# Performance work log

Hardware: AMD Instinct MI355X
Metric: run time of the kernel (lower is better)

## Reference

```python
import jax, jax.numpy as jnp
import numpy as np
import math

HEADS = 8
HID = 32
MODES = 8
IN_CH = 4
SEQ = 32
B = 2
H = 64
W = 64


def spectral_conv(x, wr, wi):
    # x: [N, Cin, H, W]; w: [Cin, Cout, m, m] complex (low rfft2 modes only)
    n, _, h, w = x.shape
    m = wr.shape[2]
    xf = jnp.fft.rfft2(x)  # [N, Cin, H, W//2+1] complex64
    of = jnp.einsum('bixy,ioxy->boxy', xf[:, :, :m, :m], wr + 1j * wi)
    out_ft = jnp.zeros((n, wr.shape[1], h, w // 2 + 1), dtype=of.dtype)
    out_ft = out_ft.at[:, :, :m, :m].set(of)
    return jnp.fft.irfft2(out_ft, s=(h, w))


def conv1x1(x, w, b):
    # x: [N, Cin, H, W], w: [Cout, Cin], b: [Cout]
    return jnp.einsum('bchw,oc->bohw', x, w) + b[None, :, None, None]


def setup_inputs() -> dict:
    key = jax.random.key(0)
    ks = jax.random.split(key, 16)
    hd = HEADS * HID
    s = 0.02
    inp = {
        'v': jax.random.normal(ks[0], (B, SEQ, IN_CH, H, W), dtype=jnp.float32),
        'qwr': jax.random.normal(ks[1], (IN_CH, hd, MODES, MODES), dtype=jnp.float32) * s,
        'qwi': jax.random.normal(ks[2], (IN_CH, hd, MODES, MODES), dtype=jnp.float32) * s,
        'kwr': jax.random.normal(ks[3], (IN_CH, hd, MODES, MODES), dtype=jnp.float32) * s,
        'kwi': jax.random.normal(ks[4], (IN_CH, hd, MODES, MODES), dtype=jnp.float32) * s,
        'vwr': jax.random.normal(ks[5], (IN_CH, hd, MODES, MODES), dtype=jnp.float32) * s,
        'vwi': jax.random.normal(ks[6], (IN_CH, hd, MODES, MODES), dtype=jnp.float32) * s,
        'u1wr': jax.random.normal(ks[7], (hd, HID, MODES, MODES), dtype=jnp.float32) * s,
        'u1wi': jax.random.normal(ks[8], (hd, HID, MODES, MODES), dtype=jnp.float32) * s,
        'u2wr': jax.random.normal(ks[9], (HID, IN_CH, MODES, MODES), dtype=jnp.float32) * s,
        'u2wi': jax.random.normal(ks[10], (HID, IN_CH, MODES, MODES), dtype=jnp.float32) * s,
        's1w': jax.random.normal(ks[11], (HID, hd), dtype=jnp.float32) * s,
        's1b': jnp.zeros((HID,), dtype=jnp.float32),
        's2w': jax.random.normal(ks[12], (IN_CH, HID), dtype=jnp.float32) * s,
        's2b': jnp.zeros((IN_CH,), dtype=jnp.float32),
    }
    return inp


def reference(v, qwr, qwi, kwr, kwi, vwr, vwi, u1wr, u1wi, u2wr, u2wi, s1w, s1b, s2w, s2b):
    b, s, c, h, w = v.shape
    scale = 1.0 / math.sqrt(HID / HEADS)
    vr = v.reshape(b * s, c, h, w)
    embed = (b, HEADS, s, -1, h, w)  # same raw row-major reshape as torch
    q = spectral_conv(vr, qwr, qwi).reshape(embed)
    k = spectral_conv(vr, kwr, kwi).reshape(embed)
    val = spectral_conv(vr, vwr, vwi).reshape(embed)
    # inner products over channel dim, then dx^2-weighted spatial integral
    ip = jnp.einsum('bhsdrc,bhtdrc->bhstrc', q, k) * scale
    dx = 1.0 / h
    l2 = jnp.sum(ip, axis=(-2, -1)) * (dx * dx)  # [b, h, s1, s2]
    A = jax.nn.softmax(l2, axis=-1)
    u = jnp.einsum('bhst,bhtdrc->bhsdrc', A, val)
    u = jnp.transpose(u, (0, 2, 1, 3, 4, 5)).reshape(b * s, HEADS * u.shape[3], h, w)
    # SimpleFNO: gelu(conv1) + skip1, then conv2 + skip2
    x1 = jax.nn.gelu(spectral_conv(u, u1wr, u1wi), approximate=False) + conv1x1(u, s1w, s1b)
    x2 = spectral_conv(x1, u2wr, u2wi) + conv1x1(x1, s2w, s2b)
    return x2.reshape(b, s, c, h, w)
```

## Files before the change

### kernel.cpp

```cpp
#include <hip/hip_runtime.h>
#include <math.h>

#define HEADS 8
#define HIDC  32
#define MODES 8
#define IN_CH 4
#define SEQ   32
#define NS    64
#define HD    256
#define NM    64
#define NPIX  4096
#define TWO_PI_D 6.283185307179586476925286766559

__device__ __forceinline__ float2 f2(float a, float b){ return make_float2(a,b); }

__global__ void twiddle_kernel(float2* __restrict__ Etab){
  int t = threadIdx.x;
  int a = t >> 3, b = t & 7;
  double sv, cv; sincos(TWO_PI_D * ((a*b) & 63) / 64.0, &sv, &cv);
  Etab[t] = f2((float)cv, (float)sv);
}

__global__ __launch_bounds__(256) void fwd_dft_kernel(const float* __restrict__ src,
                                                      const float2* __restrict__ Etab,
                                                      float2* __restrict__ dst){
  int f = blockIdx.x, tid = threadIdx.x;
  __shared__ float  s_fld[64*68];
  __shared__ float2 s_e[64][8];
  __shared__ float2 s_a1[64][8];
  for (int e = tid; e < 512; e += 256) ((float2*)s_e)[e] = Etab[e];
  const float4* f4 = (const float4*)(src + (size_t)f*NPIX);
  for (int k = tid; k < 1024; k += 256){
    float4 v = f4[k];
    int y = k >> 4, x4 = (k & 15)*4;
    float* row = &s_fld[y*68 + x4];
    row[0]=v.x; row[1]=v.y; row[2]=v.z; row[3]=v.w;
  }
  __syncthreads();
  for (int o = tid; o < 512; o += 256){
    int y = o >> 3, kx = o & 7;
    const float4* row = (const float4*)&s_fld[y*68];
    float sr = 0.f, si = 0.f;
    for (int x4 = 0; x4 < 16; ++x4){
      float4 v = row[x4];
      int xb = x4*4;
      float2 c0 = s_e[xb+0][kx], c1 = s_e[xb+1][kx];
      float2 c2 = s_e[xb+2][kx], c3 = s_e[xb+3][kx];
      sr += v.x*c0.x + v.y*c1.x + v.z*c2.x + v.w*c3.x;
      si -= v.x*c0.y + v.y*c1.y + v.z*c2.y + v.w*c3.y;
    }
    s_a1[y][kx] = f2(sr, si);
  }
  __syncthreads();
  if (tid < 64){
    int ky = tid >> 3, kx = tid & 7;
    float sr = 0.f, si = 0.f;
    for (int y = 0; y < 64; ++y){
      float2 a = s_a1[y][kx];
      float2 cs = s_e[y][ky];
      sr += a.x*cs.x + a.y*cs.y;
      si += a.y*cs.x - a.x*cs.y;
    }
    dst[(size_t)f*NM + tid] = f2(sr, si);
  }
}

__global__ __launch_bounds__(256) void gram_kernel(const float* __restrict__ qwr, const float* __restrict__ qwi,
                                                   const float* __restrict__ kwr, const float* __restrict__ kwi,
                                                   float2* __restrict__ G2, float* __restrict__ Gdc){
  int m = blockIdx.x, tid = threadIdx.x;
  __shared__ float qsr[4][257], qsi[4][257], ksr[4][257], ksi[4][257];
  for (int k = tid; k < 1024; k += 256){
    int i = k >> 8, c = k & 255;
    size_t a = ((size_t)(i*256 + c))*64 + m;
    qsr[i][c] = qwr[a]; qsi[i][c] = qwi[a];
    ksr[i][c] = kwr[a]; ksi[i][c] = kwi[a];
  }
  __syncthreads();
  int kx = m & 7, ky = m >> 3;
  float w = (kx >= 1) ? 2.0f : ((ky >= 1) ? 0.5f : 0.0f);
  for (int e = tid; e < 1024; e += 256){
    int P = e >> 7, T = (e >> 4) & 7, i = (e >> 2) & 3, j = e & 3;
    float grr=0.f, gri=0.f, gir=0.f, gii=0.f;
    for (int d = 0; d < 32; ++d){
      float ar = qsr[i][P*32+d], ai = qsi[i][P*32+d];
      float br = ksr[j][T*32+d], bi = ksi[j][T*32+d];
      grr += ar*br; gri += ar*bi; gir += ai*br; gii += ai*bi;
    }
    G2[(size_t)(((m*8+P)*4+i)*4+j)*8 + T] = f2(w*(grr+gii), w*(gir-gri));
    if (m == 0){
      int o = ((P*4+i)*4+j)*8 + T;
      Gdc[o] = grr; Gdc[1024+o] = gri; Gdc[2048+o] = gir; Gdc[3072+o] = gii;
    }
  }
}

__global__ __launch_bounds__(256) void attn_kernel(const float2* __restrict__ Vf,
                                                   const float2* __restrict__ G2,
                                                   const float* __restrict__ Gdc,
                                                   float* __restrict__ A){
  int bx = blockIdx.x;
  int s = bx & 31;
  int base = ((bx >> 8) * 32) + (((bx >> 5) & 7) * 4);
  int tid = threadIdx.x;
  int t = tid & 31, mc = tid >> 5;
  __shared__ float2 s_vf[4][IN_CH][64];
  __shared__ float  s_part[8][33];
  for (int k = tid; k < 4*IN_CH*64; k += 256){
    int m = k & 63, c = (k>>6)&3, smp = k>>8;
    s_vf[smp][c][m] = Vf[((size_t)(base+smp)*IN_CH + c)*NM + m];
  }
  __syncthreads();
  int sg = s >> 3, P = s & 7;
  int tg = t >> 3, T = t & 7;
  float acc = 0.f;
  for (int mm = 0; mm < 8; ++mm){
    int m = mc*8 + mm;
    const float2* g = G2 + (size_t)((m*8+P)*16)*8 + T;
    float sub = 0.f;
    for (int i = 0; i < 4; ++i){
      float2 a = s_vf[sg][i][m];
      for (int j = 0; j < 4; ++j){
        float2 b = s_vf[tg][j][m];
        float zr = a.x*b.x + a.y*b.y;
        float zi = a.y*b.x - a.x*b.y;
        float2 gv = g[(size_t)(i*4+j)*8];
        sub += zr*gv.x - zi*gv.y;
      }
    }
    acc += sub;
  }
  if (mc == 0){
    float sub = 0.f;
    for (int i = 0; i < 4; ++i){
      float2 a = s_vf[sg][i][0];
      for (int j = 0; j < 4; ++j){
        float2 b = s_vf[tg][j][0];
        int o = ((P*4+i)*4+j)*8 + T;
        sub += a.x*b.x*Gdc[o] - a.x*b.y*Gdc[1024+o]
             - a.y*b.x*Gdc[2048+o] + a.y*b.y*Gdc[3072+o];
      }
    }
    acc += sub;
  }
  s_part[mc][t] = acc;
  __syncthreads();
  if (tid < 32){
    float l2 = 0.f;
    for (int k = 0; k < 8; ++k) l2 += s_part[k][tid];
    l2 *= 0.5f / (4096.0f * 4096.0f);
    float mx = l2;
    for (int off = 16; off; off >>= 1) mx = fmaxf(mx, __shfl_xor(mx, off, 32));
    float e = expf(l2 - mx);
    float sm = e;
    for (int off = 16; off; off >>= 1) sm += __shfl_xor(sm, off, 32);
    A[(size_t)bx*32 + tid] = e / sm;
  }
}

__global__ __launch_bounds__(256) void uspec_kernel(const float2* __restrict__ Vf,
                                                    const float* __restrict__ vwr, const float* __restrict__ vwi,
                                                    const float* __restrict__ A,
                                                    float2* __restrict__ Uf){
  int bid = blockIdx.x;
  int mg = bid & 31, hh = (bid >> 5) & 7, b = bid >> 8;
  int m0 = mg*2;
  int nbase = b*32 + hh*4;
  int tid = threadIdx.x;
  __shared__ float2 s_vw[4][2][256];
  __shared__ float2 s_vv[4][2][256];
  __shared__ float  s_A[32][33];
  __shared__ float2 s_vf[4][4][2];
  for (int k = tid; k < 2048; k += 256){
    int i = k >> 9, mm = (k >> 8) & 1, c = k & 255;
    size_t a = ((size_t)i*256 + c)*64 + m0 + mm;
    s_vw[i][mm][c] = f2(vwr[a], vwi[a]);
  }
  for (int k = tid; k < 1024; k += 256)
    s_A[k>>5][k&31] = A[(size_t)((b*8+hh)*32 + (k>>5))*32 + (k&31)];
  if (tid < 32){
    int smp = tid >> 3, i = (tid >> 1) & 3, mm = tid & 1;
    s_vf[smp][i][mm] = Vf[((size_t)(nbase+smp)*4 + i)*64 + m0 + mm];
  }
  __syncthreads();
  for (int k = tid; k < 2048; k += 256){
    int smp = k >> 9, mm = (k >> 8) & 1, c = k & 255;
    float sr = 0.f, si = 0.f;
    for (int i = 0; i < 4; ++i){
      float2 v = s_vf[smp][i][mm];
      float2 w = s_vw[i][mm][c];
      sr += v.x*w.x - v.y*w.y;
      si += v.x*w.y + v.y*w.x;
    }
    s_vv[smp][mm][c] = f2(sr, si);
  }
  __syncthreads();
  int sg = tid >> 5, d = tid & 31;
  float2 acc[4][2];
  for (int ss = 0; ss < 4; ++ss)
    for (int mm = 0; mm < 2; ++mm) acc[ss][mm] = f2(0.f, 0.f);
  for (int tt = 0; tt < 32; ++tt){
    int tg = tt >> 3, c = (tt & 7)*32 + d;
    float a0 = s_A[sg*4+0][tt], a1 = s_A[sg*4+1][tt];
    float a2 = s_A[sg*4+2][tt], a3 = s_A[sg*4+3][tt];
    for (int mm = 0; mm < 2; ++mm){
      float2 v = s_vv[tg][mm][c];
      acc[0][mm].x += a0*v.x; acc[0][mm].y += a0*v.y;
      acc[1][mm].x += a1*v.x; acc[1][mm].y += a1*v.y;
      acc[2][mm].x += a2*v.x; acc[2][mm].y += a2*v.y;
      acc[3][mm].x += a3*v.x; acc[3][mm].y += a3*v.y;
    }
  }
  for (int ss = 0; ss < 4; ++ss){
    int n = b*32 + sg*4 + ss;
    for (int mm = 0; mm < 2; ++mm)
      Uf[((size_t)n*64 + m0 + mm)*256 + hh*32 + d] = acc[ss][mm];
  }
}

__global__ __launch_bounds__(256) void u1t_kernel(const float* __restrict__ u1wr,
                                                  const float* __restrict__ u1wi,
                                                  float4* __restrict__ u1wT){
  int t = blockIdx.x*256 + threadIdx.x;
  int o1 = t & 31, c = (t>>5) & 255, m = t >> 13;
  float pr = ((m & 7)==0 && m) ? 0.5f : 1.0f;
  float pi = m ? pr : 0.0f;
  size_t src = ((size_t)c*32 + o1)*64 + m;
  float wr = u1wr[src], wi = u1wi[src];
  u1wT[t] = make_float4(pr*wr, pi*wi, pr*wi, pi*wr);
}

__global__ __launch_bounds__(128) void mix1_kernel(const float2* __restrict__ Uf,
                                                   const float4* __restrict__ u1wT,
                                                   const float* __restrict__ s1w,
                                                   float2* __restrict__ U1f, float2* __restrict__ S1f){
  int n = blockIdx.x >> 4, mg = blockIdx.x & 15, m0 = mg*4;
  int tid = threadIdx.x;
  __shared__ float2 s_u[4][256];
  for (int k = tid; k < 1024; k += 128){
    int mm = k >> 8, c = k & 255;
    s_u[mm][c] = Uf[((size_t)n*64 + m0 + mm)*256 + c];
  }
  __syncthreads();
  int o1 = tid & 31, mm = tid >> 5;
  int m = m0 + mm;
  const float4* wp = u1wT + (size_t)m*256*32 + o1;
  const float* swp = s1w + o1*256;
  float2 au = f2(0.f,0.f), asv = f2(0.f,0.f);
  #pragma unroll 8
  for (int c = 0; c < 256; ++c){
    float2 u = s_u[mm][c];
    float4 w = wp[(size_t)c*32];
    float sw = swp[c];
    au.x  += u.x*w.x - u.y*w.y;
    au.y  += u.x*w.z + u.y*w.w;
    asv.x += u.x*sw;
    asv.y += u.y*sw;
  }
  size_t ob = ((size_t)n*32 + o1)*64 + m;
  U1f[ob] = au; S1f[ob] = asv;
}

__global__ __launch_bounds__(256) void xg_kernel(const float2* __restrict__ Etab,
                                                 const float2* __restrict__ U1f,
                                                 float2* __restrict__ Xg){
  int f = blockIdx.x, tid = threadIdx.x;
  __shared__ float2 s_e[64][8];
  __shared__ float2 s_gu[64];
  __shared__ float2 s_tu[64][8];
  __shared__ float  s_fld[64*68];
  __shared__ float2 s_a1[64][8];
  for (int e = tid; e < 512; e += 256) ((float2*)s_e)[e] = Etab[e];
  if (tid < 64) s_gu[tid] = U1f[(size_t)f*NM + tid];
  __syncthreads();
  for (int o = tid; o < 512; o += 256){
    int y = o >> 3, kx = o & 7;
    float wf = (kx ? 2.0f : 1.0f) * (1.0f/4096.0f);
    float ar=0.f, ai=0.f;
    for (int ky = 0; ky < 8; ++ky){
      float2 cs = s_e[y][ky];
      float2 gu = s_gu[ky*8+kx];
      ar += gu.x*cs.x - gu.y*cs.y;
      ai += gu.x*cs.y + gu.y*cs.x;
    }
    s_tu[y][kx] = f2(ar*wf, ai*wf);
  }
  __syncthreads();
  int xx = tid & 63;
  float2 ce[8];
  #pragma unroll
  for (int k = 0; k < 8; ++k) ce[k] = s_e[xx][k];
  for (int i = 0; i < 16; ++i){
    int p = i*256 + tid;
    int y = p >> 6;
    const float4* tp = (const float4*)&s_tu[y][0];
    float4 t0 = tp[0], t1 = tp[1], t2 = tp[2], t3 = tp[3];
    float vu = t0.x*ce[0].x - t0.y*ce[0].y + t0.z*ce[1].x - t0.w*ce[1].y
             + t1.x*ce[2].x - t1.y*ce[2].y + t1.z*ce[3].x - t1.w*ce[3].y
             + t2.x*ce[4].x - t2.y*ce[4].y + t2.z*ce[5].x - t2.w*ce[5].y
             + t3.x*ce[6].x - t3.y*ce[6].y + t3.z*ce[7].x - t3.w*ce[7].y;
    float g = 0.5f * vu * (1.0f + erff(vu * 0.70710678f));
    s_fld[y*68 + xx] = g;
  }
  __syncthreads();
  for (int o = tid; o < 512; o += 256){
    int y = o >> 3, kx = o & 7;
    const float4* row = (const float4*)&s_fld[y*68];
    float sr = 0.f, si = 0.f;
    for (int x4 = 0; x4 < 16; ++x4){
      float4 v = row[x4];
      int xb = x4*4;
      float2 c0 = s_e[xb+0][kx], c1 = s_e[xb+1][kx];
      float2 c2 = s_e[xb+2][kx], c3 = s_e[xb+3][kx];
      sr += v.x*c0.x + v.y*c1.x + v.z*c2.x + v.w*c3.x;
      si -= v.x*c0.y + v.y*c1.y + v.z*c2.y + v.w*c3.y;
    }
    s_a1[y][kx] = f2(sr, si);
  }
  __syncthreads();
  if (tid < 64){
    int ky = tid >> 3, kx = tid & 7;
    float sr = 0.f, si = 0.f;
    for (int y = 0; y < 64; ++y){
      float2 a = s_a1[y][kx];
      float2 cs = s_e[y][ky];
      sr += a.x*cs.x + a.y*cs.y;
      si += a.y*cs.x - a.x*cs.y;
    }
    Xg[(size_t)f*NM + tid] = f2(sr, si);
  }
}

__global__ __launch_bounds__(256) void final_kernel(const float2* __restrict__ Etab,
                                                    const float2* __restrict__ U1f,
                                                    const float2* __restrict__ S1f,
                                                    const float2* __restrict__ Xg,
                                                    const float* __restrict__ u2wr, const float* __restrict__ u2wi,
                                                    const float* __restrict__ s1b,
                                                    const float* __restrict__ s2w, const float* __restrict__ s2b,
                                                    float* __restrict__ out){
  int n = blockIdx.x >> 4, tile = blockIdx.x & 15, y0 = tile*4;
  int tid = threadIdx.x;
  __shared__ float2 s_e[64][8];
  __shared__ float2 s_u1[32][64];
  __shared__ float2 s_T[32][4][8];
  __shared__ float2 s_os[4][64];
  __shared__ float2 s_tmp[4][4][8];
  __shared__ float  s_w2[128], s_s1b[32], s_b2[4];
  for (int e = tid; e < 512; e += 256) ((float2*)s_e)[e] = Etab[e];
  for (int k = tid; k < 2048; k += 256) ((float2*)s_u1)[k] = U1f[(size_t)n*2048 + k];
  if (tid < 128) s_w2[tid] = s2w[tid];
  else if (tid < 160) s_s1b[tid-128] = s1b[tid-128];
  else if (tid < 164) s_b2[tid-160] = s2b[tid-160];
  __syncthreads();
  for (int e = tid; e < 1024; e += 256){
    int c = e >> 5, yy = (e >> 3) & 3, kx = e & 7;
    int y = y0 + yy;
    float wf = (kx ? 2.0f : 1.0f) * (1.0f/4096.0f);
    float ar = 0.f, ai = 0.f;
    for (int ky = 0; ky < 8; ++ky){
      float2 cs = s_e[y][ky];
      float2 g = s_u1[c][ky*8+kx];
      ar += g.x*cs.x - g.y*cs.y;
      ai += g.x*cs.y + g.y*cs.x;
    }
    s_T[c][yy][kx] = f2(ar*wf, ai*wf);
  }
  {
    int o2 = tid >> 6, m = tid & 63;
    float prm = ((m & 7)==0 && m) ? 0.5f : 1.0f;
    float pim = m ? prm : 0.0f;
    float dc = (m == 0) ? 4096.0f : 0.0f;
    float cr = 0.f, ci = 0.f;
    for (int o1 = 0; o1 < 32; ++o1){
      float2 xg = Xg[((size_t)n*32 + o1)*NM + m];
      float2 sf = S1f[((size_t)n*32 + o1)*NM + m];
      float Xr = xg.x + sf.x*prm + dc*s_s1b[o1];
      float Xi = xg.y + sf.y*pim;
      size_t wb = ((size_t)(o1*IN_CH + o2))*NM + m;
      float wr = u2wr[wb], wi = u2wi[wb];
      float sw = s_w2[o2*32 + o1];
      cr += Xr*wr - Xi*wi + sw*sf.x;
      ci += Xr*wi + Xi*wr + sw*sf.y;
    }
    s_os[o2][m] = f2(cr, ci);
  }
  __syncthreads();
  if (tid < 128){
    int o2 = tid >> 5, yy = (tid >> 3) & 3, kx = tid & 7;
    int y = y0 + yy;
    float wf = (kx ? 2.0f : 1.0f) * (1.0f/4096.0f);
    float tr=0.f, ti=0.f;
    for (int ky = 0; ky < 8; ++ky){
      float2 cs = s_e[y][ky];
      float2 g = s_os[o2][ky*8+kx];
      tr += g.x*cs.x - g.y*cs.y;
      ti += g.x*cs.y + g.y*cs.x;
    }
    s_tmp[o2][yy][kx] = f2(tr*wf, ti*wf);
  }
  __syncthreads();
  int yy = tid >> 6, xx = tid & 63;
  float2 ce[8];
  #pragma unroll
  for (int k = 0; k < 8; ++k) ce[k] = s_e[xx][k];
  float a0 = s_b2[0], a1 = s_b2[1], a2 = s_b2[2], a3 = s_b2[3];
  for (int c = 0; c < 32; ++c){
    float b = s_s1b[c];
    a0 += s_w2[c]*b; a1 += s_w2[32+c]*b; a2 += s_w2[64+c]*b; a3 += s_w2[96+c]*b;
  }
  for (int c = 0; c < 32; ++c){
    const float4* tp = (const float4*)&s_T[c][yy][0];
    float4 t0 = tp[0], t1 = tp[1], t2 = tp[2], t3 = tp[3];
    float vu = t0.x*ce[0].x - t0.y*ce[0].y + t0.z*ce[1].x - t0.w*ce[1].y
             + t1.x*ce[2].x - t1.y*ce[2].y + t1.z*ce[3].x - t1.w*ce[3].y
             + t2.x*ce[4].x - t2.y*ce[4].y + t2.z*ce[5].x - t2.w*ce[5].y
             + t3.x*ce[6].x - t3.y*ce[6].y + t3.z*ce[7].x - t3.w*ce[7].y;
    float g = 0.5f * vu * (1.0f + erff(vu * 0.70710678f));
    a0 += s_w2[c]*g; a1 += s_w2[32+c]*g; a2 += s_w2[64+c]*g; a3 += s_w2[96+c]*g;
  }
  float sp[4];
  #pragma unroll
  for (int o2 = 0; o2 < 4; ++o2){
    const float4* tp = (const float4*)&s_tmp[o2][yy][0];
    float4 t0 = tp[0], t1 = tp[1], t2 = tp[2], t3 = tp[3];
    sp[o2] = t0.x*ce[0].x - t0.y*ce[0].y + t0.z*ce[1].x - t0.w*ce[1].y
           + t1.x*ce[2].x - t1.y*ce[2].y + t1.z*ce[3].x - t1.w*ce[3].y
           + t2.x*ce[4].x - t2.y*ce[4].y + t2.z*ce[5].x - t2.w*ce[5].y
           + t3.x*ce[6].x - t3.y*ce[6].y + t3.z*ce[7].x - t3.w*ce[7].y;
  }
  int p = (y0 + yy)*64 + xx;
  float* ob = out + (size_t)n*IN_CH*NPIX;
  ob[p]          = a0 + sp[0];
  ob[NPIX + p]   = a1 + sp[1];
  ob[2*NPIX + p] = a2 + sp[2];
  ob[3*NPIX + p] = a3 + sp[3];
}

extern "C" void kernel_launch(void* const* d_in, const int* in_sizes, int n_in,
                              void* d_out, int out_size, void* d_ws, size_t ws_size,
                              hipStream_t stream) {
  (void)in_sizes; (void)n_in; (void)out_size; (void)ws_size;
  const float* v    = (const float*)d_in[0];
  const float* qwr  = (const float*)d_in[1];
  const float* qwi  = (const float*)d_in[2];
  const float* kwr  = (const float*)d_in[3];
  const float* kwi  = (const float*)d_in[4];
  const float* vwr  = (const float*)d_in[5];
  const float* vwi  = (const float*)d_in[6];
  const float* u1wr = (const float*)d_in[7];
  const float* u1wi = (const float*)d_in[8];
  const float* u2wr = (const float*)d_in[9];
  const float* u2wi = (const float*)d_in[10];
  const float* s1w  = (const float*)d_in[11];
  const float* s1b  = (const float*)d_in[12];
  const float* s2w  = (const float*)d_in[13];
  const float* s2b  = (const float*)d_in[14];
  float* out = (float*)d_out;

  float* ws = (float*)d_ws;
  size_t off = 0;
  float2* Etab =(float2*)(ws + off); off += 1024;
  float2* Vf   = (float2*)(ws + off); off += (size_t)NS*IN_CH*NM*2;
  float2* G2   = (float2*)(ws + off); off += (size_t)65536*2;
  float*  Gdc  =          (ws + off); off += 4096;
  float*  A    =          (ws + off); off += 16384;
  float2* Uf   = (float2*)(ws + off); off += (size_t)NS*NM*HD*2;
  float2* U1f  = (float2*)(ws + off); off += (size_t)NS*HIDC*NM*2;
  float2* S1f  = (float2*)(ws + off); off += (size_t)NS*HIDC*NM*2;
  float2* Xg   = (float2*)(ws + off); off += (size_t)NS*HIDC*NM*2;
  float4* u1wT = (float4*)(ws + off); off += (size_t)524288*4;

  twiddle_kernel<<<1, 512, 0, stream>>>(Etab);
  fwd_dft_kernel<<<NS*IN_CH, 256, 0, stream>>>(v, Etab, Vf);
  gram_kernel<<<64, 256, 0, stream>>>(qwr, qwi, kwr, kwi, G2, Gdc);
  u1t_kernel<<<2048, 256, 0, stream>>>(u1wr, u1wi, u1wT);
  attn_kernel<<<512, 256, 0, stream>>>(Vf, G2, Gdc, A);
  uspec_kernel<<<512, 256, 0, stream>>>(Vf, vwr, vwi, A, Uf);
  mix1_kernel<<<1024, 128, 0, stream>>>(Uf, u1wT, s1w, U1f, S1f);
  xg_kernel<<<NS*HIDC, 256, 0, stream>>>(Etab, U1f, Xg);
  final_kernel<<<NS*16, 256, 0, stream>>>(Etab, U1f, S1f, Xg, u2wr, u2wi, s1b, s2w, s2b, out);
}
```

Baseline: 222.0 us.

## Batch samples in mix1/xg, pre-transpose value weights, coalesce u1 transpose

mix1 now processes four samples per block, so each u1 weight load is reused across four samples and the grid shrinks fourfold. xg handles two fields per block, sharing the twiddle load and reusing the s_tu buffer for the stage-one DFT output. A new v1t kernel transposes the value spectral weights so uspec loads them contiguously, and u1t now reads coalesced instead of writing coalesced. fwd_dft uses 512 threads with one output per thread. The trade-offs are fewer blocks and higher register and shared-memory use per block, plus one extra small launch.

```diff
diff --git a/kernel.cpp b/kernel.cpp
--- a/kernel.cpp
+++ b/kernel.cpp
@@ -21,23 +21,24 @@
   Etab[t] = f2((float)cv, (float)sv);
 }
 
-__global__ __launch_bounds__(256) void fwd_dft_kernel(const float* __restrict__ src,
+__global__ __launch_bounds__(512) void fwd_dft_kernel(const float* __restrict__ src,
                                                       const float2* __restrict__ Etab,
                                                       float2* __restrict__ dst){
   int f = blockIdx.x, tid = threadIdx.x;
   __shared__ float  s_fld[64*68];
   __shared__ float2 s_e[64][8];
   __shared__ float2 s_a1[64][8];
-  for (int e = tid; e < 512; e += 256) ((float2*)s_e)[e] = Etab[e];
+  if (tid < 512) ((float2*)s_e)[tid] = Etab[tid];
   const float4* f4 = (const float4*)(src + (size_t)f*NPIX);
-  for (int k = tid; k < 1024; k += 256){
+  for (int k = tid; k < 1024; k += 512){
     float4 v = f4[k];
     int y = k >> 4, x4 = (k & 15)*4;
     float* row = &s_fld[y*68 + x4];
     row[0]=v.x; row[1]=v.y; row[2]=v.z; row[3]=v.w;
   }
   __syncthreads();
-  for (int o = tid; o < 512; o += 256){
+  {
+    int o = tid;
     int y = o >> 3, kx = o & 7;
     const float4* row = (const float4*)&s_fld[y*68];
     float sr = 0.f, si = 0.f;
@@ -158,8 +159,16 @@
   }
 }
 
+__global__ __launch_bounds__(256) void v1t_kernel(const float* __restrict__ vwr,
+                                                  const float* __restrict__ vwi,
+                                                  float2* __restrict__ vwT){
+  int t = blockIdx.x*256 + threadIdx.x;
+  int m = t & 63, r = t >> 6, i = r >> 8, c = r & 255;
+  vwT[((size_t)m*256 + c)*4 + i] = f2(vwr[t], vwi[t]);
+}
+
 __global__ __launch_bounds__(256) void uspec_kernel(const float2* __restrict__ Vf,
-                                                    const float* __restrict__ vwr, const float* __restrict__ vwi,
+                                                    const float2* __restrict__ vwT,
                                                     const float* __restrict__ A,
                                                     float2* __restrict__ Uf){
   int bid = blockIdx.x;
@@ -172,9 +181,8 @@
   __shared__ float  s_A[32][33];
   __shared__ float2 s_vf[4][4][2];
   for (int k = tid; k < 2048; k += 256){
-    int i = k >> 9, mm = (k >> 8) & 1, c = k & 255;
-    size_t a = ((size_t)i*256 + c)*64 + m0 + mm;
-    s_vw[i][mm][c] = f2(vwr[a], vwi[a]);
+    int mm = k >> 10, c = (k >> 2) & 255, i = k & 3;
+    s_vw[i][mm][c] = vwT[(size_t)m0*1024 + k];
   }
   for (int k = tid; k < 1024; k += 256)
     s_A[k>>5][k&31] = A[(size_t)((b*8+hh)*32 + (k>>5))*32 + (k&31)];
@@ -222,90 +230,105 @@
                                                   const float* __restrict__ u1wi,
                                                   float4* __restrict__ u1wT){
   int t = blockIdx.x*256 + threadIdx.x;
-  int o1 = t & 31, c = (t>>5) & 255, m = t >> 13;
+  int m = t & 63, r = t >> 6, c = r >> 5, o1 = r & 31;
   float pr = ((m & 7)==0 && m) ? 0.5f : 1.0f;
   float pi = m ? pr : 0.0f;
-  size_t src = ((size_t)c*32 + o1)*64 + m;
-  float wr = u1wr[src], wi = u1wi[src];
-  u1wT[t] = make_float4(pr*wr, pi*wi, pr*wi, pi*wr);
+  float wr = u1wr[t], wi = u1wi[t];
+  u1wT[((size_t)m*256 + c)*32 + o1] = make_float4(pr*wr, pi*wi, pr*wi, pi*wr);
 }
 
 __global__ __launch_bounds__(128) void mix1_kernel(const float2* __restrict__ Uf,
                                                    const float4* __restrict__ u1wT,
                                                    const float* __restrict__ s1w,
                                                    float2* __restrict__ U1f, float2* __restrict__ S1f){
-  int n = blockIdx.x >> 4, mg = blockIdx.x & 15, m0 = mg*4;
+  int bid = blockIdx.x;
+  int n0 = (bid >> 4)*4, mg = bid & 15, m0 = mg*4;
   int tid = threadIdx.x;
-  __shared__ float2 s_u[4][256];
-  for (int k = tid; k < 1024; k += 128){
-    int mm = k >> 8, c = k & 255;
-    s_u[mm][c] = Uf[((size_t)n*64 + m0 + mm)*256 + c];
+  __shared__ float2 s_u[4][4][256];
+  for (int k = tid; k < 4096; k += 128){
+    int smp = k >> 10, mm = (k >> 8) & 3, c = k & 255;
+    s_u[smp][mm][c] = Uf[((size_t)(n0+smp)*64 + m0 + mm)*256 + c];
   }
   __syncthreads();
   int o1 = tid & 31, mm = tid >> 5;
   int m = m0 + mm;
-  const float4* wp = u1wT + (size_t)m*256*32 + o1;
+  const float4* wp = u1wT + (size_t)m*8192 + o1;
   const float* swp = s1w + o1*256;
-  float2 au = f2(0.f,0.f), asv = f2(0.f,0.f);
-  #pragma unroll 8
+  float2 au[4], asv[4];
+  #pragma unroll
+  for (int s = 0; s < 4; ++s){ au[s] = f2(0.f,0.f); asv[s] = f2(0.f,0.f); }
   for (int c = 0; c < 256; ++c){
-    float2 u = s_u[mm][c];
     float4 w = wp[(size_t)c*32];
     float sw = swp[c];
-    au.x  += u.x*w.x - u.y*w.y;
-    au.y  += u.x*w.z + u.y*w.w;
-    asv.x += u.x*sw;
-    asv.y += u.y*sw;
-  }
-  size_t ob = ((size_t)n*32 + o1)*64 + m;
-  U1f[ob] = au; S1f[ob] = asv;
+    #pragma unroll
+    for (int s = 0; s < 4; ++s){
+      float2 u = s_u[s][mm][c];
+      au[s].x  += u.x*w.x - u.y*w.y;
+      au[s].y  += u.x*w.z + u.y*w.w;
+      asv[s].x += u.x*sw;
+      asv[s].y += u.y*sw;
+    }
+  }
+  #pragma unroll
+  for (int s = 0; s < 4; ++s){
+    size_t ob = ((size_t)(n0+s)*32 + o1)*64 + m;
+    U1f[ob] = au[s]; S1f[ob] = asv[s];
+  }
 }
 
 __global__ __launch_bounds__(256) void xg_kernel(const float2* __restrict__ Etab,
                                                  const float2* __restrict__ U1f,
                                                  float2* __restrict__ Xg){
-  int f = blockIdx.x, tid = threadIdx.x;
+  int f0 = blockIdx.x*2, tid = threadIdx.x;
   __shared__ float2 s_e[64][8];
-  __shared__ float2 s_gu[64];
-  __shared__ float2 s_tu[64][8];
-  __shared__ float  s_fld[64*68];
-  __shared__ float2 s_a1[64][8];
+  __shared__ float2 s_gu[2][64];
+  __shared__ float2 s_tu[2][64][8];
+  __shared__ float  s_fld[2][64*68];
   for (int e = tid; e < 512; e += 256) ((float2*)s_e)[e] = Etab[e];
-  if (tid < 64) s_gu[tid] = U1f[(size_t)f*NM + tid];
-  __syncthreads();
-  for (int o = tid; o < 512; o += 256){
-    int y = o >> 3, kx = o & 7;
+  if (tid < 128) ((float2*)s_gu)[tid] = U1f[(size_t)f0*NM + tid];
+  __syncthreads();
+  for (int o = tid; o < 1024; o += 256){
+    int fl = o >> 9, r = o & 511, y = r >> 3, kx = r & 7;
     float wf = (kx ? 2.0f : 1.0f) * (1.0f/4096.0f);
     float ar=0.f, ai=0.f;
     for (int ky = 0; ky < 8; ++ky){
       float2 cs = s_e[y][ky];
-      float2 gu = s_gu[ky*8+kx];
+      float2 gu = s_gu[fl][ky*8+kx];
       ar += gu.x*cs.x - gu.y*cs.y;
       ai += gu.x*cs.y + gu.y*cs.x;
     }
-    s_tu[y][kx] = f2(ar*wf, ai*wf);
+    s_tu[fl][y][kx] = f2(ar*wf, ai*wf);
   }
   __syncthreads();
   int xx = tid & 63;
   float2 ce[8];
   #pragma unroll
   for (int k = 0; k < 8; ++k) ce[k] = s_e[xx][k];
+  #pragma unroll 2
   for (int i = 0; i < 16; ++i){
-    int p = i*256 + tid;
-    int y = p >> 6;
-    const float4* tp = (const float4*)&s_tu[y][0];
-    float4 t0 = tp[0], t1 = tp[1], t2 = tp[2], t3 = tp[3];
-    float vu = t0.x*ce[0].x - t0.y*ce[0].y + t0.z*ce[1].x - t0.w*ce[1].y
-             + t1.x*ce[2].x - t1.y*ce[2].y + t1.z*ce[3].x - t1.w*ce[3].y
-             + t2.x*ce[4].x - t2.y*ce[4].y + t2.z*ce[5].x - t2.w*ce[5].y
-             + t3.x*ce[6].x - t3.y*ce[6].y + t3.z*ce[7].x - t3.w*ce[7].y;
-    float g = 0.5f * vu * (1.0f + erff(vu * 0.70710678f));
-    s_fld[y*68 + xx] = g;
-  }
-  __syncthreads();
-  for (int o = tid; o < 512; o += 256){
-    int y = o >> 3, kx = o & 7;
-    const float4* row = (const float4*)&s_fld[y*68];
+    int p = i*256 + tid, y = p >> 6;
+    const float4* tp0 = (const float4*)&s_tu[0][y][0];
+    const float4* tp1 = (const float4*)&s_tu[1][y][0];
+    float4 a0=tp0[0], a1=tp0[1], a2=tp0[2], a3=tp0[3];
+    float4 b0=tp1[0], b1=tp1[1], b2=tp1[2], b3=tp1[3];
+    float v0 = a0.x*ce[0].x - a0.y*ce[0].y + a0.z*ce[1].x - a0.w*ce[1].y
+             + a1.x*ce[2].x - a1.y*ce[2].y + a1.z*ce[3].x - a1.w*ce[3].y
+             + a2.x*ce[4].x - a2.y*ce[4].y + a2.z*ce[5].x - a2.w*ce[5].y
+             + a3.x*ce[6].x - a3.y*ce[6].y + a3.z*ce[7].x - a3.w*ce[7].y;
+    float v1 = b0.x*ce[0].x - b0.y*ce[0].y + b0.z*ce[1].x - b0.w*ce[1].y
+             + b1.x*ce[2].x - b1.y*ce[2].y + b1.z*ce[3].x - b1.w*ce[3].y
+             + b2.x*ce[4].x - b2.y*ce[4].y + b2.z*ce[5].x - b2.w*ce[5].y
+             + b3.x*ce[6].x - b3.y*ce[6].y + b3.z*ce[7].x - b3.w*ce[7].y;
+    float g0 = 0.5f * v0 * (1.0f + erff(v0 * 0.70710678f));
+    float g1 = 0.5f * v1 * (1.0f + erff(v1 * 0.70710678f));
+    s_fld[0][y*68 + xx] = g0;
+    s_fld[1][y*68 + xx] = g1;
+  }
+  __syncthreads();
+  float2 (*s_a1)[64][8] = s_tu;
+  for (int o = tid; o < 1024; o += 256){
+    int fl = o >> 9, r = o & 511, y = r >> 3, kx = r & 7;
+    const float4* row = (const float4*)&s_fld[fl][y*68];
     float sr = 0.f, si = 0.f;
     for (int x4 = 0; x4 < 16; ++x4){
       float4 v = row[x4];
@@ -315,19 +338,20 @@
       sr += v.x*c0.x + v.y*c1.x + v.z*c2.x + v.w*c3.x;
       si -= v.x*c0.y + v.y*c1.y + v.z*c2.y + v.w*c3.y;
     }
-    s_a1[y][kx] = f2(sr, si);
-  }
-  __syncthreads();
-  if (tid < 64){
-    int ky = tid >> 3, kx = tid & 7;
+    s_a1[fl][y][kx] = f2(sr, si);
+  }
+  __syncthreads();
+  if (tid < 128){
+    int fl = tid >> 6, t6 = tid & 63;
+    int ky = t6 >> 3, kx = t6 & 7;
     float sr = 0.f, si = 0.f;
     for (int y = 0; y < 64; ++y){
-      float2 a = s_a1[y][kx];
+      float2 a = s_a1[fl][y][kx];
       float2 cs = s_e[y][ky];
       sr += a.x*cs.x + a.y*cs.y;
       si += a.y*cs.x - a.x*cs.y;
     }
-    Xg[(size_t)f*NM + tid] = f2(sr, si);
+    Xg[(size_t)(f0+fl)*NM + t6] = f2(sr, si);
   }
 }
 
@@ -470,14 +494,16 @@
   float2* S1f  = (float2*)(ws + off); off += (size_t)NS*HIDC*NM*2;
   float2* Xg   = (float2*)(ws + off); off += (size_t)NS*HIDC*NM*2;
   float4* u1wT = (float4*)(ws + off); off += (size_t)524288*4;
+  float2* vwT  = (float2*)(ws + off); off += (size_t)65536*2;
 
   twiddle_kernel<<<1, 512, 0, stream>>>(Etab);
-  fwd_dft_kernel<<<NS*IN_CH, 256, 0, stream>>>(v, Etab, Vf);
+  fwd_dft_kernel<<<NS*IN_CH, 512, 0, stream>>>(v, Etab, Vf);
   gram_kernel<<<64, 256, 0, stream>>>(qwr, qwi, kwr, kwi, G2, Gdc);
   u1t_kernel<<<2048, 256, 0, stream>>>(u1wr, u1wi, u1wT);
+  v1t_kernel<<<256, 256, 0, stream>>>(vwr, vwi, vwT);
   attn_kernel<<<512, 256, 0, stream>>>(Vf, G2, Gdc, A);
-  uspec_kernel<<<512, 256, 0, stream>>>(Vf, vwr, vwi, A, Uf);
-  mix1_kernel<<<1024, 128, 0, stream>>>(Uf, u1wT, s1w, U1f, S1f);
-  xg_kernel<<<NS*HIDC, 256, 0, stream>>>(Etab, U1f, Xg);
+  uspec_kernel<<<512, 256, 0, stream>>>(Vf, vwT, A, Uf);
+  mix1_kernel<<<256, 128, 0, stream>>>(Uf, u1wT, s1w, U1f, S1f);
+  xg_kernel<<<1024, 256, 0, stream>>>(Etab, U1f, Xg);
   final_kernel<<<NS*16, 256, 0, stream>>>(Etab, U1f, S1f, Xg, u2wr, u2wi, s1b, s2w, s2b, out);
 }
```

Result: slower. 240.4 us (+8.3%).
